# Kernel optimization log

Measured on AMD Instinct MI355X. Metric: run time of the kernel, lower is better.

## Reference

```python
import jax, jax.numpy as jnp
import numpy as np
from jax import lax

EPS = 1e-5
DN = ('NCHW', 'OIHW', 'NCHW')


def ternarize(w):
    # Standard TWN-style ternarization: {-1, 0, +1} with threshold 0.7*mean|w|
    thr = 0.7 * jnp.mean(jnp.abs(w))
    return jnp.sign(w) * (jnp.abs(w) > thr).astype(w.dtype)


def conv(x, w, b=None):
    y = lax.conv_general_dilated(x, w, (1, 1), 'VALID', dimension_numbers=DN)
    if b is not None:
        y = y + b[None, :, None, None]
    return y


def bn(x, g, be, m, v):
    inv = g / jnp.sqrt(v + EPS)
    return x * inv[None, :, None, None] + (be - m * inv)[None, :, None, None]


def maxpool2(x):
    return lax.reduce_window(x, -jnp.inf, lax.max, (1, 1, 2, 2), (1, 1, 2, 2), 'VALID')


def setup_inputs() -> dict:
    key = jax.random.key(0)
    ks = jax.random.split(key, 21)
    d = {}
    d['x'] = jax.random.normal(ks[0], (8192, 1, 28, 28), jnp.float32)
    d['w1'] = ternarize(jax.random.normal(ks[1], (32, 1, 5, 5), jnp.float32))
    d['b1'] = jax.random.normal(ks[2], (32,), jnp.float32) * 0.1
    d['g1'] = jax.random.uniform(ks[3], (32,), jnp.float32, 0.5, 1.5)
    d['be1'] = jax.random.normal(ks[4], (32,), jnp.float32) * 0.1
    d['m1'] = jax.random.normal(ks[5], (32,), jnp.float32) * 0.1
    d['v1'] = jax.random.uniform(ks[6], (32,), jnp.float32, 0.5, 1.5)
    d['w2'] = ternarize(jax.random.normal(ks[7], (64, 32, 5, 5), jnp.float32))
    d['b2'] = jax.random.normal(ks[8], (64,), jnp.float32) * 0.1
    d['g2'] = jax.random.uniform(ks[9], (64,), jnp.float32, 0.5, 1.5)
    d['be2'] = jax.random.normal(ks[10], (64,), jnp.float32) * 0.1
    d['m2'] = jax.random.normal(ks[11], (64,), jnp.float32) * 0.1
    d['v2'] = jax.random.uniform(ks[12], (64,), jnp.float32, 0.5, 1.5)
    d['w3'] = ternarize(jax.random.normal(ks[13], (512, 1024, 1, 1), jnp.float32))
    d['b3'] = jax.random.normal(ks[14], (512,), jnp.float32) * 0.1
    d['g3'] = jax.random.uniform(ks[15], (512,), jnp.float32, 0.5, 1.5)
    d['be3'] = jax.random.normal(ks[16], (512,), jnp.float32) * 0.1
    d['m3'] = jax.random.normal(ks[17], (512,), jnp.float32) * 0.1
    d['v3'] = jax.random.uniform(ks[18], (512,), jnp.float32, 0.5, 1.5)
    d['w4'] = jax.random.normal(ks[19], (10, 512, 1, 1), jnp.float32) * 0.05
    return d


def reference(x, w1, b1, g1, be1, m1, v1, w2, b2, g2, be2, m2, v2,
              w3, b3, g3, be3, m3, v3, w4):
    h = conv(x, w1, b1)                       # [B,32,24,24]
    h = maxpool2(jax.nn.relu(bn(h, g1, be1, m1, v1)))   # [B,32,12,12]
    h = conv(h, w2, b2)                       # [B,64,8,8]
    h = maxpool2(jax.nn.relu(bn(h, g2, be2, m2, v2)))   # [B,64,4,4]
    h = h.reshape(-1, 1024, 1, 1)             # flatten C,H,W
    h = jax.nn.relu(bn(conv(h, w3, b3), g3, be3, m3, v3))  # [B,512,1,1]
    h = conv(h, w4)                            # [B,10,1,1]
    return h.reshape(-1, 10)
```

## Files before the change

### kernel.cpp

```cpp
#include <hip/hip_runtime.h>

#define EPS 1e-5f

typedef float f32x4 __attribute__((ext_vector_type(4)));
typedef short short8_t __attribute__((ext_vector_type(8)));
typedef unsigned int uint4v __attribute__((ext_vector_type(4)));
typedef unsigned short ushort_t;

__global__ void prep_kernel(const float* __restrict__ b1, const float* __restrict__ g1,
                            const float* __restrict__ be1, const float* __restrict__ m1,
                            const float* __restrict__ v1,
                            const float* __restrict__ b2, const float* __restrict__ g2,
                            const float* __restrict__ be2, const float* __restrict__ m2,
                            const float* __restrict__ v2,
                            const float* __restrict__ b3, const float* __restrict__ g3,
                            const float* __restrict__ be3, const float* __restrict__ m3,
                            const float* __restrict__ v3,
                            const float* __restrict__ w1, const float* __restrict__ w2,
                            const float* __restrict__ w3,
                            ushort_t* __restrict__ w1frag, ushort_t* __restrict__ w2frag,
                            ushort_t* __restrict__ w3frag, float* __restrict__ prm) {
  int tid = blockIdx.x * blockDim.x + threadIdx.x;
  int stride = gridDim.x * blockDim.x;
  for (int c = tid; c < 32; c += stride) {
    float s = g1[c] / sqrtf(v1[c] + EPS);
    prm[c] = s;
    prm[32 + c] = (b1[c] - m1[c]) * s + be1[c];
  }
  for (int c = tid; c < 64; c += stride) {
    float s = g2[c] / sqrtf(v2[c] + EPS);
    prm[64 + c] = s;
    prm[128 + c] = (b2[c] - m2[c]) * s + be2[c];
  }
  for (int c = tid; c < 512; c += stride) {
    float s = g3[c] / sqrtf(v3[c] + EPS);
    prm[192 + c] = s;
    prm[704 + c] = (b3[c] - m3[c]) * s + be3[c];
  }
  for (int i = tid; i < 2 * 2 * 64 * 8; i += stride) {
    const int j = i & 7;
    const int l = (i >> 3) & 63;
    const int nt = (i >> 9) & 1;
    const int p = i >> 10;
    const int oc = nt * 16 + (l & 15);
    const int t = (l >> 4) * 8 + j;
    const float v = (t < 25) ? w1[oc * 25 + t] : 0.f;
    const unsigned u = __float_as_uint(v);
    const ushort_t hi = (ushort_t)(u >> 16);
    const float r = v - __uint_as_float(u & 0xffff0000u);
    const ushort_t lo = (ushort_t)(__float_as_uint(r) >> 16);
    w1frag[i] = p ? lo : hi;
  }
  for (int i = tid; i < 25 * 4 * 64 * 8; i += stride) {
    const int kk = i >> 11;
    const int r = i & 2047;
    const int nt = r >> 9;
    const int r2 = r & 511;
    const int l = r2 >> 3;
    const int j = r2 & 7;
    const int oc = nt * 16 + (l & 15);
    const int ic = (l >> 4) * 8 + j;
    w2frag[i] = (ushort_t)(__float_as_uint(w2[oc * 800 + ic * 25 + kk]) >> 16);
  }
  for (int i = tid; i < 32 * 32 * 64 * 8; i += stride) {
    const int ks = i >> 14;
    const int r = i & 16383;
    const int ntg = r >> 9;
    const int r2 = r & 511;
    const int l = r2 >> 3;
    const int j = r2 & 7;
    const int oc = ntg * 16 + (l & 15);
    const int k = ks * 32 + (l >> 4) * 8 + j;
    w3frag[i] = (ushort_t)(__float_as_uint(w3[oc * 1024 + k]) >> 16);
  }
}

__launch_bounds__(128)
__global__ void conv12_kernel(const float* __restrict__ x,
                              const ushort_t* __restrict__ w1frag,
                              const ushort_t* __restrict__ w2frag,
                              const float* __restrict__ prm,
                              ushort_t* __restrict__ h2pH, ushort_t* __restrict__ h2pL) {
  __shared__ __align__(16) unsigned char lds[26240];

  const int tid = threadIdx.x;
  const int w = tid >> 6, l = tid & 63;
  const int b = blockIdx.x;
  const int m15 = l & 15, g = l >> 4;

  float* imgf = (float*)lds;
  ushort_t* insA = (ushort_t*)(lds + 3200);

  const float* xb = x + (size_t)b * 784;
  for (int i = tid; i < 196; i += 128) ((float4*)imgf)[i] = ((const float4*)xb)[i];
  if (tid < 16) imgf[784 + tid] = 0.f;

  short8_t B1h[2], B1l[2];
#pragma unroll
  for (int nt = 0; nt < 2; ++nt) {
    B1h[nt] = *(const short8_t*)(w1frag + (size_t)(nt * 64 + l) * 8);
    B1l[nt] = *(const short8_t*)(w1frag + (size_t)((2 + nt) * 64 + l) * 8);
  }

  int off[8];
#pragma unroll
  for (int j = 0; j < 8; ++j) {
    const int t = g * 8 + j;
    const int ky = t / 5, kx = t - ky * 5;
    off[j] = (t < 25) ? (ky * 28 + kx) : 0;
  }

  float s1[2], sh1[2], s2[4], sh2[4];
#pragma unroll
  for (int nt = 0; nt < 2; ++nt) {
    s1[nt] = prm[nt * 16 + m15];
    sh1[nt] = prm[32 + nt * 16 + m15];
  }
#pragma unroll
  for (int nt = 0; nt < 4; ++nt) {
    s2[nt] = prm[64 + nt * 16 + m15];
    sh2[nt] = prm[128 + nt * 16 + m15];
  }
  __syncthreads();

#pragma unroll 1
  for (int i = 0; i < 18; ++i) {
    const int mt = w * 18 + i;
    const int q = mt * 16 + m15;
    const int p_pool = q >> 2, sub = q & 3;
    const int py = p_pool / 12, px = p_pool - py * 12;
    const int Y = 2 * py + (sub >> 1), X = 2 * px + (sub & 1);
    const float* pixb = imgf + Y * 28 + X;
    float v[8];
#pragma unroll
    for (int j = 0; j < 8; ++j) v[j] = pixb[off[j]];
    uint4v hv, lv;
#pragma unroll
    for (int k = 0; k < 4; ++k) {
      const unsigned u0 = __float_as_uint(v[2 * k]);
      const unsigned u1 = __float_as_uint(v[2 * k + 1]);
      hv[k] = (u0 >> 16) | (u1 & 0xffff0000u);
      const float r0 = v[2 * k] - __uint_as_float(u0 & 0xffff0000u);
      const float r1 = v[2 * k + 1] - __uint_as_float(u1 & 0xffff0000u);
      lv[k] = (__float_as_uint(r0) >> 16) | (__float_as_uint(r1) & 0xffff0000u);
    }
    const short8_t ah = __builtin_bit_cast(short8_t, hv);
    const short8_t al = __builtin_bit_cast(short8_t, lv);

    f32x4 c0 = {0.f, 0.f, 0.f, 0.f}, c1 = {0.f, 0.f, 0.f, 0.f};
    c0 = __builtin_amdgcn_mfma_f32_16x16x32_bf16(ah, B1h[0], c0, 0, 0, 0);
    c1 = __builtin_amdgcn_mfma_f32_16x16x32_bf16(ah, B1h[1], c1, 0, 0, 0);
    c0 = __builtin_amdgcn_mfma_f32_16x16x32_bf16(al, B1h[0], c0, 0, 0, 0);
    c1 = __builtin_amdgcn_mfma_f32_16x16x32_bf16(al, B1h[1], c1, 0, 0, 0);
    c0 = __builtin_amdgcn_mfma_f32_16x16x32_bf16(ah, B1l[0], c0, 0, 0, 0);
    c1 = __builtin_amdgcn_mfma_f32_16x16x32_bf16(ah, B1l[1], c1, 0, 0, 0);

    const int cell = mt * 4 + g;
#pragma unroll
    for (int nt = 0; nt < 2; ++nt) {
      const f32x4 c = nt ? c1 : c0;
      const float pv = fmaxf(fmaxf(c[0], c[1]), fmaxf(c[2], c[3]));
      const float a = fmaxf(fmaf(pv, s1[nt], sh1[nt]), 0.f);
      const unsigned u = __float_as_uint(a);
      const float r = a - __uint_as_float(u & 0xffff0000u);
      const int ic = nt * 16 + m15;
      insA[cell * 40 + ic] = (ushort_t)(u >> 16);
      insA[5760 + cell * 40 + ic] = (ushort_t)(__float_as_uint(r) >> 16);
    }
  }
  __syncthreads();

  const int sy = (m15 & 3) >> 1, sx = m15 & 1;
  const int X2 = 2 * (m15 >> 2) + sx;

  f32x4 acc[2][4];
#pragma unroll
  for (int m = 0; m < 2; ++m)
#pragma unroll
    for (int nt = 0; nt < 4; ++nt) acc[m][nt] = (f32x4){0.f, 0.f, 0.f, 0.f};

#pragma unroll 1
  for (int pass = 0; pass < 5; ++pass) {
    short8_t wr[5][4];
#pragma unroll
    for (int kx = 0; kx < 5; ++kx)
#pragma unroll
      for (int nt = 0; nt < 4; ++nt)
        wr[kx][nt] = *(const short8_t*)(w2frag + (size_t)(((pass * 5 + kx) * 4 + nt) * 64 + l) * 8);
#pragma unroll
    for (int kx = 0; kx < 5; ++kx) {
#pragma unroll
      for (int m = 0; m < 2; ++m) {
        const int mt2 = 2 * w + m;
        const int cellin = (2 * mt2 + sy + pass) * 12 + X2 + kx;
        const short8_t aH = *(const short8_t*)(insA + cellin * 40 + g * 8);
        const short8_t aL = *(const short8_t*)(insA + 5760 + cellin * 40 + g * 8);
#pragma unroll
        for (int nt = 0; nt < 4; ++nt) {
          acc[m][nt] = __builtin_amdgcn_mfma_f32_16x16x32_bf16(aH, wr[kx][nt], acc[m][nt], 0, 0, 0);
          acc[m][nt] = __builtin_amdgcn_mfma_f32_16x16x32_bf16(aL, wr[kx][nt], acc[m][nt], 0, 0, 0);
        }
      }
    }
  }

  const size_t ob = (size_t)b * 1024;
#pragma unroll
  for (int m = 0; m < 2; ++m) {
    const int cell2 = (2 * w + m) * 4 + g;
#pragma unroll
    for (int nt = 0; nt < 4; ++nt) {
      const f32x4 c = acc[m][nt];
      const float pv = fmaxf(fmaxf(c[0], c[1]), fmaxf(c[2], c[3]));
      const float a = fmaxf(fmaf(pv, s2[nt], sh2[nt]), 0.f);
      const unsigned u = __float_as_uint(a);
      const float r = a - __uint_as_float(u & 0xffff0000u);
      const int oc = nt * 16 + m15;
      h2pH[ob + oc * 16 + cell2] = (ushort_t)(u >> 16);
      h2pL[ob + oc * 16 + cell2] = (ushort_t)(__float_as_uint(r) >> 16);
    }
  }
}

__launch_bounds__(256)
__global__ void fc3_kernel(const ushort_t* __restrict__ h2pH, const ushort_t* __restrict__ h2pL,
                           const ushort_t* __restrict__ w3frag, const float* __restrict__ prm,
                           float* __restrict__ a3) {
  const int orig = blockIdx.x + (blockIdx.y << 3);
  const int xcd = orig & 7;
  const int j = orig >> 3;
  const int ytile = (xcd << 4) | (j >> 3);
  const int xtile = j & 7;
  const int n0 = xtile * 64;
  const int m0 = ytile * 64;
  const int w = threadIdx.x >> 6, l = threadIdx.x & 63;
  const int mrow = m0 + w * 16 + (l & 15);
  const int kc8 = (l >> 4) * 8;

  const ushort_t* aHp = h2pH + (size_t)mrow * 1024 + kc8;
  const ushort_t* aLp = h2pL + (size_t)mrow * 1024 + kc8;
  const ushort_t* bp = w3frag + (size_t)(n0 >> 4) * 512 + (size_t)l * 8;

  f32x4 accH[4], accL[4];
#pragma unroll
  for (int t = 0; t < 4; ++t) {
    accH[t] = (f32x4){0.f, 0.f, 0.f, 0.f};
    accL[t] = (f32x4){0.f, 0.f, 0.f, 0.f};
  }

#pragma unroll 2
  for (int ks = 0; ks < 32; ++ks) {
    const short8_t aH = *(const short8_t*)(aHp + ks * 32);
    const short8_t aL = *(const short8_t*)(aLp + ks * 32);
    const ushort_t* bks = bp + (size_t)ks * 16384;
#pragma unroll
    for (int t = 0; t < 4; ++t) {
      const short8_t bb = *(const short8_t*)(bks + t * 512);
      accH[t] = __builtin_amdgcn_mfma_f32_16x16x32_bf16(aH, bb, accH[t], 0, 0, 0);
      accL[t] = __builtin_amdgcn_mfma_f32_16x16x32_bf16(aL, bb, accL[t], 0, 0, 0);
    }
  }

#pragma unroll
  for (int t = 0; t < 4; ++t) {
    const int oc = n0 + t * 16 + (l & 15);
    const float s = prm[192 + oc], sh = prm[704 + oc];
#pragma unroll
    for (int r = 0; r < 4; ++r) {
      const int m = m0 + w * 16 + (l >> 4) * 4 + r;
      a3[(size_t)m * 512 + oc] = fmaxf(fmaf(accH[t][r] + accL[t][r], s, sh), 0.f);
    }
  }
}

__launch_bounds__(256)
__global__ void fc4_kernel(const float* __restrict__ a3, const float* __restrict__ w4,
                           float* __restrict__ out, int B) {
  const int w = threadIdx.x >> 6, l = threadIdx.x & 63;
  const int b = blockIdx.x * 4 + w;
  if (b >= B) return;
  const float4* ar = (const float4*)(a3 + (size_t)b * 512);
  const float4 a0 = ar[l * 2];
  const float4 a1 = ar[l * 2 + 1];
#pragma unroll
  for (int j = 0; j < 10; ++j) {
    const float4* wr = (const float4*)(w4 + j * 512);
    const float4 w0 = wr[l * 2];
    const float4 w1 = wr[l * 2 + 1];
    float sv = a0.x * w0.x + a0.y * w0.y + a0.z * w0.z + a0.w * w0.w +
               a1.x * w1.x + a1.y * w1.y + a1.z * w1.z + a1.w * w1.w;
#pragma unroll
    for (int off = 1; off < 64; off <<= 1) sv += __shfl_xor(sv, off);
    if (l == 0) out[(size_t)b * 10 + j] = sv;
  }
}

extern "C" void kernel_launch(void* const* d_in, const int* in_sizes, int n_in,
                              void* d_out, int out_size, void* d_ws, size_t ws_size,
                              hipStream_t stream) {
  const float* x  = (const float*)d_in[0];
  const float* w1 = (const float*)d_in[1];
  const float* b1 = (const float*)d_in[2];
  const float* g1 = (const float*)d_in[3];
  const float* be1 = (const float*)d_in[4];
  const float* m1 = (const float*)d_in[5];
  const float* v1 = (const float*)d_in[6];
  const float* w2 = (const float*)d_in[7];
  const float* b2 = (const float*)d_in[8];
  const float* g2 = (const float*)d_in[9];
  const float* be2 = (const float*)d_in[10];
  const float* m2 = (const float*)d_in[11];
  const float* v2 = (const float*)d_in[12];
  const float* w3 = (const float*)d_in[13];
  const float* b3 = (const float*)d_in[14];
  const float* g3 = (const float*)d_in[15];
  const float* be3 = (const float*)d_in[16];
  const float* m3 = (const float*)d_in[17];
  const float* v3 = (const float*)d_in[18];
  const float* w4 = (const float*)d_in[19];

  const int B = in_sizes[0] / 784;

  float* prm = (float*)d_ws;
  ushort_t* w1frag = (ushort_t*)(prm + 1216);
  ushort_t* w2frag = w1frag + 2048;
  ushort_t* w3frag = w2frag + 51200;
  ushort_t* h2pH = w3frag + 524288;
  ushort_t* h2pL = h2pH + (size_t)B * 1024;
  float* a3 = (float*)(h2pL + (size_t)B * 1024);

  prep_kernel<<<64, 256, 0, stream>>>(b1, g1, be1, m1, v1, b2, g2, be2, m2, v2,
                                      b3, g3, be3, m3, v3, w1, w2, w3,
                                      w1frag, w2frag, w3frag, prm);
  conv12_kernel<<<B, 128, 0, stream>>>(x, w1frag, w2frag, prm, h2pH, h2pL);
  dim3 g3d(8, B / 64);
  fc3_kernel<<<g3d, 256, 0, stream>>>(h2pH, h2pL, w3frag, prm, a3);
  fc4_kernel<<<(B + 3) / 4, 256, 0, stream>>>(a3, w4, (float*)d_out, B);
}
```

Before: 283.1 us.

## Pre-split input into bf16 hi/lo once, widen fc3 tile, merge accumulators

```diff
diff --git a/kernel.cpp b/kernel.cpp
--- a/kernel.cpp
+++ b/kernel.cpp
@@ -88,12 +88,17 @@
   const int b = blockIdx.x;
   const int m15 = l & 15, g = l >> 4;
 
-  float* imgf = (float*)lds;
+  unsigned* imgP = (unsigned*)lds;
   ushort_t* insA = (ushort_t*)(lds + 3200);
 
   const float* xb = x + (size_t)b * 784;
-  for (int i = tid; i < 196; i += 128) ((float4*)imgf)[i] = ((const float4*)xb)[i];
-  if (tid < 16) imgf[784 + tid] = 0.f;
+  for (int i = tid; i < 784; i += 128) {
+    const float v = xb[i];
+    const unsigned u = __float_as_uint(v);
+    const float r = v - __uint_as_float(u & 0xffff0000u);
+    imgP[i] = (u & 0xffff0000u) | (__float_as_uint(r) >> 16);
+  }
+  if (tid < 16) imgP[784 + tid] = 0u;
 
   short8_t B1h[2], B1l[2];
 #pragma unroll
@@ -130,19 +135,15 @@
     const int p_pool = q >> 2, sub = q & 3;
     const int py = p_pool / 12, px = p_pool - py * 12;
     const int Y = 2 * py + (sub >> 1), X = 2 * px + (sub & 1);
-    const float* pixb = imgf + Y * 28 + X;
-    float v[8];
-#pragma unroll
-    for (int j = 0; j < 8; ++j) v[j] = pixb[off[j]];
+    const unsigned* pixb = imgP + Y * 28 + X;
+    unsigned pv[8];
+#pragma unroll
+    for (int j = 0; j < 8; ++j) pv[j] = pixb[off[j]];
     uint4v hv, lv;
 #pragma unroll
     for (int k = 0; k < 4; ++k) {
-      const unsigned u0 = __float_as_uint(v[2 * k]);
-      const unsigned u1 = __float_as_uint(v[2 * k + 1]);
-      hv[k] = (u0 >> 16) | (u1 & 0xffff0000u);
-      const float r0 = v[2 * k] - __uint_as_float(u0 & 0xffff0000u);
-      const float r1 = v[2 * k + 1] - __uint_as_float(u1 & 0xffff0000u);
-      lv[k] = (__float_as_uint(r0) >> 16) | (__float_as_uint(r1) & 0xffff0000u);
+      hv[k] = (pv[2 * k] >> 16) | (pv[2 * k + 1] & 0xffff0000u);
+      lv[k] = (pv[2 * k] & 0xffffu) | (pv[2 * k + 1] << 16);
     }
     const short8_t ah = __builtin_bit_cast(short8_t, hv);
     const short8_t al = __builtin_bit_cast(short8_t, lv);
@@ -159,8 +160,8 @@
 #pragma unroll
     for (int nt = 0; nt < 2; ++nt) {
       const f32x4 c = nt ? c1 : c0;
-      const float pv = fmaxf(fmaxf(c[0], c[1]), fmaxf(c[2], c[3]));
-      const float a = fmaxf(fmaf(pv, s1[nt], sh1[nt]), 0.f);
+      const float pvv = fmaxf(fmaxf(c[0], c[1]), fmaxf(c[2], c[3]));
+      const float a = fmaxf(fmaf(pvv, s1[nt], sh1[nt]), 0.f);
       const unsigned u = __float_as_uint(a);
       const float r = a - __uint_as_float(u & 0xffff0000u);
       const int ic = nt * 16 + m15;
@@ -211,8 +212,8 @@
 #pragma unroll
     for (int nt = 0; nt < 4; ++nt) {
       const f32x4 c = acc[m][nt];
-      const float pv = fmaxf(fmaxf(c[0], c[1]), fmaxf(c[2], c[3]));
-      const float a = fmaxf(fmaf(pv, s2[nt], sh2[nt]), 0.f);
+      const float pvv = fmaxf(fmaxf(c[0], c[1]), fmaxf(c[2], c[3]));
+      const float a = fmaxf(fmaf(pvv, s2[nt], sh2[nt]), 0.f);
       const unsigned u = __float_as_uint(a);
       const float r = a - __uint_as_float(u & 0xffff0000u);
       const int oc = nt * 16 + m15;
@@ -226,12 +227,12 @@
 __global__ void fc3_kernel(const ushort_t* __restrict__ h2pH, const ushort_t* __restrict__ h2pL,
                            const ushort_t* __restrict__ w3frag, const float* __restrict__ prm,
                            float* __restrict__ a3) {
-  const int orig = blockIdx.x + (blockIdx.y << 3);
+  const int orig = blockIdx.x + (blockIdx.y << 2);
   const int xcd = orig & 7;
   const int j = orig >> 3;
-  const int ytile = (xcd << 4) | (j >> 3);
-  const int xtile = j & 7;
-  const int n0 = xtile * 64;
+  const int ytile = (xcd << 4) | (j >> 2);
+  const int xtile = j & 3;
+  const int n0 = xtile * 128;
   const int m0 = ytile * 64;
   const int w = threadIdx.x >> 6, l = threadIdx.x & 63;
   const int mrow = m0 + w * 16 + (l & 15);
@@ -241,12 +242,9 @@
   const ushort_t* aLp = h2pL + (size_t)mrow * 1024 + kc8;
   const ushort_t* bp = w3frag + (size_t)(n0 >> 4) * 512 + (size_t)l * 8;
 
-  f32x4 accH[4], accL[4];
-#pragma unroll
-  for (int t = 0; t < 4; ++t) {
-    accH[t] = (f32x4){0.f, 0.f, 0.f, 0.f};
-    accL[t] = (f32x4){0.f, 0.f, 0.f, 0.f};
-  }
+  f32x4 acc[8];
+#pragma unroll
+  for (int t = 0; t < 8; ++t) acc[t] = (f32x4){0.f, 0.f, 0.f, 0.f};
 
 #pragma unroll 2
   for (int ks = 0; ks < 32; ++ks) {
@@ -254,21 +252,21 @@
     const short8_t aL = *(const short8_t*)(aLp + ks * 32);
     const ushort_t* bks = bp + (size_t)ks * 16384;
 #pragma unroll
-    for (int t = 0; t < 4; ++t) {
+    for (int t = 0; t < 8; ++t) {
       const short8_t bb = *(const short8_t*)(bks + t * 512);
-      accH[t] = __builtin_amdgcn_mfma_f32_16x16x32_bf16(aH, bb, accH[t], 0, 0, 0);
-      accL[t] = __builtin_amdgcn_mfma_f32_16x16x32_bf16(aL, bb, accL[t], 0, 0, 0);
-    }
-  }
-
-#pragma unroll
-  for (int t = 0; t < 4; ++t) {
+      acc[t] = __builtin_amdgcn_mfma_f32_16x16x32_bf16(aH, bb, acc[t], 0, 0, 0);
+      acc[t] = __builtin_amdgcn_mfma_f32_16x16x32_bf16(aL, bb, acc[t], 0, 0, 0);
+    }
+  }
+
+#pragma unroll
+  for (int t = 0; t < 8; ++t) {
     const int oc = n0 + t * 16 + (l & 15);
     const float s = prm[192 + oc], sh = prm[704 + oc];
 #pragma unroll
     for (int r = 0; r < 4; ++r) {
       const int m = m0 + w * 16 + (l >> 4) * 4 + r;
-      a3[(size_t)m * 512 + oc] = fmaxf(fmaf(accH[t][r] + accL[t][r], s, sh), 0.f);
+      a3[(size_t)m * 512 + oc] = fmaxf(fmaf(acc[t][r], s, sh), 0.f);
     }
   }
 }
@@ -329,11 +327,11 @@
   ushort_t* h2pL = h2pH + (size_t)B * 1024;
   float* a3 = (float*)(h2pL + (size_t)B * 1024);
 
-  prep_kernel<<<64, 256, 0, stream>>>(b1, g1, be1, m1, v1, b2, g2, be2, m2, v2,
-                                      b3, g3, be3, m3, v3, w1, w2, w3,
-                                      w1frag, w2frag, w3frag, prm);
+  prep_kernel<<<256, 256, 0, stream>>>(b1, g1, be1, m1, v1, b2, g2, be2, m2, v2,
+                                       b3, g3, be3, m3, v3, w1, w2, w3,
+                                       w1frag, w2frag, w3frag, prm);
   conv12_kernel<<<B, 128, 0, stream>>>(x, w1frag, w2frag, prm, h2pH, h2pL);
-  dim3 g3d(8, B / 64);
+  dim3 g3d(4, B / 64);
   fc3_kernel<<<g3d, 256, 0, stream>>>(h2pH, h2pL, w3frag, prm, a3);
   fc4_kernel<<<(B + 3) / 4, 256, 0, stream>>>(a3, w4, (float*)d_out, B);
 }
```

After: 262.7 us. -7.2%, faster.
